# Kernel tuning notes

Measured on AMD Instinct MI355X. Metric: run time of the kernel, lower is better.

Reference implementation:

```python
import jax, jax.numpy as jnp
import numpy as np

N_USER = 100000
N_ITEM = 100000
SUPP = 10000
B = 1024
L = 50
S = 256
H = 4
E = 64
HID = 64


def setup_inputs() -> dict:
    key = jax.random.key(0)
    ks = jax.random.split(key, 32)
    f32 = jnp.float32
    inp = {}
    # forward int args
    inp["x"] = jax.random.randint(ks[0], (B, 2), 0, N_USER)
    inp["src_his"] = jax.random.randint(ks[1], (B, L), 0, N_ITEM)
    inp["src_hl"] = jax.random.randint(ks[2], (B,), 0, L)
    inp["tgt_his"] = jax.random.randint(ks[3], (B, L), 0, N_ITEM)
    inp["tgt_hl"] = jax.random.randint(ks[4], (B,), 0, L)
    # precomputed neighbor sampling: [2 get_user_emb calls, H heads, B, S]
    inp["sample_idx"] = jax.random.randint(ks[5], (2, H, B, S), 0, SUPP)
    inp["supp_users"] = jax.random.randint(ks[6], (SUPP,), 0, N_USER)
    # embedding tables (xavier-ish small scale)
    inp["src_user_emb"] = jax.random.normal(ks[7], (N_USER, E), f32) * 0.1
    inp["src_item_emb"] = jax.random.normal(ks[8], (N_ITEM, E), f32) * 0.1
    inp["tgt_user_emb"] = jax.random.normal(ks[9], (N_USER, E), f32) * 0.1
    inp["tgt_item_emb"] = jax.random.normal(ks[10], (N_ITEM, E), f32) * 0.1
    # attention / aggregation weights, stored [in, out]
    s = 1.0 / np.sqrt(E)
    inp["W_att_w"] = jax.random.normal(ks[11], (E, E), f32) * s
    inp["W_att_b"] = jnp.full((E,), 0.1, f32)
    inp["W_agg_w"] = jax.random.normal(ks[12], (E, E), f32) * s
    # per-head GAT projections, batched over heads
    inp["Wq"] = jax.random.normal(ks[13], (H, E, E), f32) * s
    inp["Wk"] = jax.random.normal(ks[14], (H, E, E), f32) * s
    inp["Wv"] = jax.random.normal(ks[15], (H, E, E), f32) * s
    inp["W_out"] = jax.random.normal(ks[16], (H * E, E), f32) * (1.0 / np.sqrt(H * E))
    # scoring MLP
    inp["l1_w"] = jax.random.normal(ks[17], (2 * E, HID), f32) * (1.0 / np.sqrt(2 * E))
    inp["l1_b"] = jnp.full((HID,), 0.1, f32)
    inp["l2_w"] = jax.random.normal(ks[18], (HID, E), f32) * (1.0 / np.sqrt(HID))
    inp["l2_b"] = jnp.full((E,), 0.1, f32)
    inp["l3_w"] = jax.random.normal(ks[19], (E, 1), f32) * s
    inp["l3_b"] = jnp.full((1,), 0.1, f32)
    return inp


def reference(x, src_his, src_hl, tgt_his, tgt_hl, sample_idx, supp_users,
              src_user_emb, src_item_emb, tgt_user_emb, tgt_item_emb,
              W_att_w, W_att_b, W_agg_w, Wq, Wk, Wv, W_out,
              l1_w, l1_b, l2_w, l2_b, l3_w, l3_b):
    user_id = x[:, 0]
    item_id = x[:, 1]

    def user_fea_encode(his, hl, user_table):
        # NOTE: original always gathers from src_model.item_embedding (even for tgt)
        Lh = his.shape[1]
        valid = jnp.arange(Lh)[None, :] < hl[:, None]          # [B,L]
        hist = src_item_emb[his] * valid[..., None]             # [B,L,E], padded rows zeroed
        u = user_table[user_id]                                 # [B,E]
        keyt = jnp.tanh(hist @ W_att_w + W_att_b)               # [B,L,E]
        pad = hist.sum(-1) == 0                                 # [B,L]
        att = jnp.einsum('ble,be->bl', keyt, u)
        # faithful masked_softmax: masked scores set to 0 BEFORE exp (exp(0)=1 still contributes)
        att = jnp.where(pad, 0.0, att)
        e = jnp.exp(att)
        att = e / (jnp.sum(e, axis=1, keepdims=True) + 1e-12)
        out = jnp.einsum('bl,ble->be', att, hist)
        return out @ W_agg_w                                    # W_agg has no bias

    def get_user_emb(fea, idx):
        # idx: [H,B,S] indices into supp_users; all heads batched in one einsum chain
        neigh = tgt_user_emb[supp_users[idx]]                   # [H,B,S,E]
        q = jnp.einsum('be,heo->hbo', fea, Wq)                  # [H,B,O]
        k = jnp.einsum('hbse,heo->hbso', neigh, Wk)             # [H,B,S,O]
        attn = jax.nn.softmax(jnp.einsum('hbo,hbso->hbs', q, k), axis=-1)
        ctx = jnp.einsum('hbs,hbso->hbo', attn, k)              # weighted sum over neighbors
        g = jnp.einsum('hbo,hop->hbp', ctx, Wv)                 # [H,B,O]
        g = jnp.transpose(g, (1, 0, 2)).reshape(fea.shape[0], -1)  # concat heads -> [B,H*O]
        return g @ W_out

    user_src_fea = user_fea_encode(src_his, src_hl, src_user_emb)
    user_emb = get_user_emb(user_src_fea, sample_idx[0])
    item_emb = tgt_item_emb[item_id]
    user_tgt_fea = user_fea_encode(tgt_his, tgt_hl, tgt_user_emb)
    hybrid_tgt_emb = get_user_emb(user_tgt_fea, sample_idx[1])

    x_t = jnp.concatenate([hybrid_tgt_emb, item_emb], axis=1)
    x1_t = jnp.tanh(x_t @ l1_w + l1_b)
    x2_t = jnp.tanh(x1_t @ l2_w + l2_b)
    x3_t = (x2_t @ l3_w + l3_b).reshape(-1)

    output = jnp.sum(user_emb * item_emb, axis=1)
    out_emb_s = user_emb * item_emb
    # (output, output_t, out_emb_s, out_emb_t); train=False branch (sim/domain heads are None)
    return (output, x3_t, out_emb_s, x2_t)
```

## Files before the change

kernel.cpp:

```cpp
#include <hip/hip_runtime.h>

constexpr int B    = 1024;
constexpr int L    = 50;
constexpr int S    = 256;
constexpr int H    = 4;
constexpr int E    = 64;
constexpr int HID  = 64;
constexpr int SUPP = 10000;

__device__ __forceinline__ float tanh_fast(float x) {
    const float xc = fminf(fmaxf(x, -15.0f), 15.0f);
    const float e  = __expf(2.0f * xc);
    return (e - 1.0f) * __builtin_amdgcn_rcpf(e + 1.0f);
}

__global__ __launch_bounds__(256) void pre_kernel(
    const int* __restrict__ x,
    const int* __restrict__ src_his,
    const int* __restrict__ src_hl,
    const int* __restrict__ tgt_his,
    const int* __restrict__ tgt_hl,
    const float* __restrict__ item_emb,
    const float* __restrict__ src_user_emb,
    const float* __restrict__ tgt_user_emb,
    const int* __restrict__ supp_users,
    const float* __restrict__ W_att_w,
    const float* __restrict__ W_att_b,
    const float* __restrict__ W_agg_w,
    const float* __restrict__ Wq,
    const float* __restrict__ Wk,
    float* __restrict__ qout,
    float* __restrict__ K_supp)
{
    const int tid  = threadIdx.x;
    const int lane = tid & 63;
    const int wave = tid >> 6;

    if (blockIdx.y == 2) {
        __shared__ __align__(16) float sEv[4][E];
        const int h = wave;
        float wkc[E];
#pragma unroll
        for (int i = 0; i < E; i++) wkc[i] = Wk[h * E * E + i * E + lane];

        for (int j0 = blockIdx.x * 4; j0 < SUPP; j0 += gridDim.x * 4) {
            const int jm = j0 + wave;
            if (jm < SUPP) {
                const int u = supp_users[jm];
                sEv[wave][lane] = tgt_user_emb[(size_t)u * E + lane];
            }
            __syncthreads();
            const int mmax = min(4, SUPP - j0);
            for (int m = 0; m < mmax; m++) {
                const float4* e4 = (const float4*)&sEv[m][0];
                float a0 = 0.0f, a1 = 0.0f, a2 = 0.0f, a3 = 0.0f;
#pragma unroll
                for (int k = 0; k < 16; k++) {
                    const float4 v = e4[k];
                    a0 += v.x * wkc[4 * k + 0];
                    a1 += v.y * wkc[4 * k + 1];
                    a2 += v.z * wkc[4 * k + 2];
                    a3 += v.w * wkc[4 * k + 3];
                }
                K_supp[((size_t)h * SUPP + j0 + m) * E + lane] = (a0 + a1) + (a2 + a3);
            }
            __syncthreads();
        }
        return;
    }

    __shared__ __align__(16) float sHist[L * E];
    __shared__ float sHs[L];
    __shared__ float sAtt[L];
    __shared__ float sPart[4][E];
    __shared__ __align__(16) float sOut[E];
    __shared__ __align__(16) float sFea[E];

    const int b    = blockIdx.x;
    const int call = blockIdx.y;

    const int* his = call ? tgt_his : src_his;
    const int* hl  = call ? tgt_hl  : src_hl;
    const float* user_table = call ? tgt_user_emb : src_user_emb;

    float wcol[E];
#pragma unroll
    for (int i = 0; i < E; i++) wcol[i] = W_att_w[i * E + lane];

    const int uid    = x[2 * b];
    const float uv   = user_table[(size_t)uid * E + lane];
    const float bias = W_att_b[lane];
    const int hlen   = hl[b];

    for (int l = wave; l < L; l += 4) {
        const int it = his[b * L + l];
        const float hv = (l < hlen) ? item_emb[(size_t)it * E + lane] : 0.0f;
        sHist[l * E + lane] = hv;
        float hs = hv;
#pragma unroll
        for (int off = 32; off; off >>= 1) hs += __shfl_xor(hs, off);
        if (lane == 0) sHs[l] = hs;
    }
    __syncthreads();

    for (int l = wave; l < L; l += 4) {
        const float4* hrow = (const float4*)&sHist[l * E];
        float a0 = 0.0f, a1 = 0.0f, a2 = 0.0f, a3 = 0.0f;
#pragma unroll
        for (int k = 0; k < 16; k++) {
            const float4 h4 = hrow[k];
            a0 += h4.x * wcol[4 * k + 0];
            a1 += h4.y * wcol[4 * k + 1];
            a2 += h4.z * wcol[4 * k + 2];
            a3 += h4.w * wcol[4 * k + 3];
        }
        float part = tanh_fast((a0 + a1) + (a2 + a3) + bias) * uv;
#pragma unroll
        for (int off = 32; off; off >>= 1) part += __shfl_xor(part, off);
        const float hs = sHs[l];
        if (lane == 0) sAtt[l] = (hs == 0.0f) ? 0.0f : part;
    }
    __syncthreads();

    if (wave == 0) {
        float v = (lane < L) ? __expf(sAtt[lane]) : 0.0f;
        float s = v;
#pragma unroll
        for (int off = 32; off; off >>= 1) s += __shfl_xor(s, off);
        const float denom = s + 1e-12f;
        if (lane < L) sAtt[lane] = v / denom;
    }
    __syncthreads();

    float c = 0.0f;
    for (int l = wave; l < L; l += 4) c += sAtt[l] * sHist[l * E + lane];
    sPart[wave][lane] = c;
    __syncthreads();
    if (tid < E) sOut[tid] = sPart[0][tid] + sPart[1][tid] + sPart[2][tid] + sPart[3][tid];
    __syncthreads();

    {
        const float4* o4 = (const float4*)&sOut[wave * 16];
        float g0 = 0.0f, g1 = 0.0f, g2 = 0.0f, g3 = 0.0f;
#pragma unroll
        for (int k = 0; k < 4; k++) {
            const float4 v = o4[k];
            const int i = wave * 16 + 4 * k;
            g0 += v.x * W_agg_w[(i + 0) * E + lane];
            g1 += v.y * W_agg_w[(i + 1) * E + lane];
            g2 += v.z * W_agg_w[(i + 2) * E + lane];
            g3 += v.w * W_agg_w[(i + 3) * E + lane];
        }
        sPart[wave][lane] = (g0 + g1) + (g2 + g3);
    }
    __syncthreads();
    if (tid < E) sFea[tid] = sPart[0][tid] + sPart[1][tid] + sPart[2][tid] + sPart[3][tid];
    __syncthreads();

    {
        const float* Wqh = Wq + wave * E * E;
        const float4* f4p = (const float4*)sFea;
        float q0 = 0.0f, q1 = 0.0f, q2 = 0.0f, q3 = 0.0f;
#pragma unroll
        for (int k = 0; k < 16; k++) {
            const float4 f4 = f4p[k];
            q0 += f4.x * Wqh[(4 * k + 0) * E + lane];
            q1 += f4.y * Wqh[(4 * k + 1) * E + lane];
            q2 += f4.z * Wqh[(4 * k + 2) * E + lane];
            q3 += f4.w * Wqh[(4 * k + 3) * E + lane];
        }
        qout[(((call * H) + wave) * B + b) * E + lane] = (q0 + q1) + (q2 + q3);
    }
}

__global__ __launch_bounds__(256) void attn_kernel(
    const int* __restrict__ sample_idx,
    const float* __restrict__ K_supp,
    const float* __restrict__ qarr,
    const float* __restrict__ Wv,
    float* __restrict__ gout)
{
    __shared__ float sRed[8];
    __shared__ float sCtx[4][E];
    __shared__ float sC[E];
    __shared__ float sG[4][E];

    const int n    = blockIdx.x;
    const int xcd  = n & 7;
    const int h    = xcd >> 1;
    const int call = xcd & 1;
    const int b    = n >> 3;
    const int tid  = threadIdx.x;
    const int lane = tid & 63;
    const int wave = tid >> 6;
    const int u    = lane & 15;
    const int rsub = lane >> 4;
    const int s0   = wave * 64;

    const int* idx = sample_idx + (((call * H) + h) * B + b) * S;
    const float* Kh = K_supp + (size_t)h * SUPP * E;
    const float4 qu = *(const float4*)(qarr + ((size_t)(((call * H) + h) * B + b)) * E + 4 * u);

    float4 kreg[16];
    float mylogit = 0.0f;
#pragma unroll
    for (int i = 0; i < 16; i++) {
        const int j = idx[s0 + 4 * i + rsub];
        kreg[i] = *(const float4*)(Kh + (size_t)j * E + 4 * u);
        float part = kreg[i].x * qu.x + kreg[i].y * qu.y
                   + kreg[i].z * qu.z + kreg[i].w * qu.w;
#pragma unroll
        for (int off = 1; off < 16; off <<= 1) part += __shfl_xor(part, off);
        mylogit = (u == i) ? part : mylogit;
    }

    float m = mylogit;
#pragma unroll
    for (int off = 32; off; off >>= 1) m = fmaxf(m, __shfl_xor(m, off));
    if (lane == 0) sRed[wave] = m;
    __syncthreads();
    const float mx = fmaxf(fmaxf(sRed[0], sRed[1]), fmaxf(sRed[2], sRed[3]));
    const float ex = __expf(mylogit - mx);
    float sm = ex;
#pragma unroll
    for (int off = 32; off; off >>= 1) sm += __shfl_xor(sm, off);
    if (lane == 0) sRed[4 + wave] = sm;
    __syncthreads();
    const float denom = sRed[4] + sRed[5] + sRed[6] + sRed[7];
    const float pval = ex / denom;

    float4 cacc = make_float4(0.0f, 0.0f, 0.0f, 0.0f);
#pragma unroll
    for (int i = 0; i < 16; i++) {
        const float p = __shfl(pval, (lane & 48) + i);
        cacc.x += p * kreg[i].x;
        cacc.y += p * kreg[i].y;
        cacc.z += p * kreg[i].z;
        cacc.w += p * kreg[i].w;
    }
#pragma unroll
    for (int off = 16; off <= 32; off <<= 1) {
        cacc.x += __shfl_xor(cacc.x, off);
        cacc.y += __shfl_xor(cacc.y, off);
        cacc.z += __shfl_xor(cacc.z, off);
        cacc.w += __shfl_xor(cacc.w, off);
    }
    if (lane < 16) *(float4*)(&sCtx[wave][u * 4]) = cacc;
    __syncthreads();
    if (wave == 0) {
        sC[lane] = sCtx[0][lane] + sCtx[1][lane] + sCtx[2][lane] + sCtx[3][lane];
    }
    __syncthreads();

    const float* Wvh = Wv + h * E * E;
    float g = 0.0f;
#pragma unroll
    for (int k = 0; k < 16; k++) {
        const int c = wave * 16 + k;
        g += sC[c] * Wvh[c * E + lane];
    }
    sG[wave][lane] = g;
    __syncthreads();
    if (wave == 0) {
        gout[((size_t)(call * B) + b) * (H * E) + h * E + lane] =
            sG[0][lane] + sG[1][lane] + sG[2][lane] + sG[3][lane];
    }
}

__global__ __launch_bounds__(256) void final_kernel(
    const int* __restrict__ x,
    const float* __restrict__ tgt_item_emb,
    const float* __restrict__ gsrc,
    const float* __restrict__ gtgt,
    const float* __restrict__ W_out,
    const float* __restrict__ l1_w,
    const float* __restrict__ l1_b,
    const float* __restrict__ l2_w,
    const float* __restrict__ l2_b,
    const float* __restrict__ l3_w,
    const float* __restrict__ l3_b,
    float* __restrict__ out)
{
    __shared__ float sPart[4][E];
    __shared__ float sHyb[E];
    __shared__ float sItem[E];
    __shared__ float sX1[HID];

    const int b    = blockIdx.x;
    const int tid  = threadIdx.x;
    const int lane = tid & 63;
    const int wave = tid >> 6;

    if (tid < E) {
        const int item = x[2 * b + 1];
        sItem[tid] = tgt_item_emb[(size_t)item * E + tid];
    }

    const float* grow = (wave < 2) ? (gsrc + (size_t)b * (H * E))
                                   : (gtgt + (size_t)b * (H * E));
    const int i0 = (wave & 1) * 128;
    {
        const float4* g4 = (const float4*)(grow + i0);
        float a0 = 0.0f, a1 = 0.0f, a2 = 0.0f, a3 = 0.0f;
#pragma unroll
        for (int k = 0; k < 32; k++) {
            const float4 v = g4[k];
            const float* wr = W_out + (i0 + 4 * k) * E + lane;
            a0 += v.x * wr[0];
            a1 += v.y * wr[E];
            a2 += v.z * wr[2 * E];
            a3 += v.w * wr[3 * E];
        }
        sPart[wave][lane] = (a0 + a1) + (a2 + a3);
    }
    __syncthreads();

    if (wave == 0) {
        const float ue = sPart[0][lane] + sPart[1][lane];
        const float prod = ue * sItem[lane];
        out[2 * B + b * E + lane] = prod;
        float s = prod;
#pragma unroll
        for (int off = 32; off; off >>= 1) s += __shfl_xor(s, off);
        if (lane == 0) out[b] = s;
    }
    if (wave == 1) {
        sHyb[lane] = sPart[2][lane] + sPart[3][lane];
    }
    __syncthreads();

    float a1 = 0.0f;
#pragma unroll
    for (int k = 0; k < 32; k++) {
        const int i = wave * 32 + k;
        const float v = (i < 64) ? sHyb[i] : sItem[i - 64];
        a1 += v * l1_w[i * HID + lane];
    }
    sPart[wave][lane] = a1;
    __syncthreads();

    if (wave == 0) {
        const float a = l1_b[lane] + sPart[0][lane] + sPart[1][lane]
                      + sPart[2][lane] + sPart[3][lane];
        sX1[lane] = tanh_fast(a);
    }
    __syncthreads();

    if (wave == 0) {
        float a = l2_b[lane];
#pragma unroll
        for (int i = 0; i < HID; i++) a += sX1[i] * l2_w[i * E + lane];
        const float x2 = tanh_fast(a);
        out[2 * B + B * E + b * E + lane] = x2;
        float p = x2 * l3_w[lane];
#pragma unroll
        for (int off = 32; off; off >>= 1) p += __shfl_xor(p, off);
        if (lane == 0) out[B + b] = p + l3_b[0];
    }
}

extern "C" void kernel_launch(void* const* d_in, const int* in_sizes, int n_in,
                              void* d_out, int out_size, void* d_ws, size_t ws_size,
                              hipStream_t stream) {
    const int*   x            = (const int*)d_in[0];
    const int*   src_his      = (const int*)d_in[1];
    const int*   src_hl       = (const int*)d_in[2];
    const int*   tgt_his      = (const int*)d_in[3];
    const int*   tgt_hl       = (const int*)d_in[4];
    const int*   sample_idx   = (const int*)d_in[5];
    const int*   supp_users   = (const int*)d_in[6];
    const float* src_user_emb = (const float*)d_in[7];
    const float* src_item_emb = (const float*)d_in[8];
    const float* tgt_user_emb = (const float*)d_in[9];
    const float* tgt_item_emb = (const float*)d_in[10];
    const float* W_att_w      = (const float*)d_in[11];
    const float* W_att_b      = (const float*)d_in[12];
    const float* W_agg_w      = (const float*)d_in[13];
    const float* Wq           = (const float*)d_in[14];
    const float* Wk           = (const float*)d_in[15];
    const float* Wv           = (const float*)d_in[16];
    const float* W_out        = (const float*)d_in[17];
    const float* l1_w         = (const float*)d_in[18];
    const float* l1_b         = (const float*)d_in[19];
    const float* l2_w         = (const float*)d_in[20];
    const float* l2_b         = (const float*)d_in[21];
    const float* l3_w         = (const float*)d_in[22];
    const float* l3_b         = (const float*)d_in[23];

    float* ws      = (float*)d_ws;
    float* qarr    = ws;
    float* K_supp  = qarr + 2 * H * B * E;
    float* garr    = K_supp + H * SUPP * E;
    float* out     = (float*)d_out;

    pre_kernel<<<dim3(B, 3), 256, 0, stream>>>(
        x, src_his, src_hl, tgt_his, tgt_hl, src_item_emb,
        src_user_emb, tgt_user_emb, supp_users,
        W_att_w, W_att_b, W_agg_w, Wq, Wk, qarr, K_supp);
    attn_kernel<<<dim3(B * H * 2), 256, 0, stream>>>(
        sample_idx, K_supp, qarr, Wv, garr);
    final_kernel<<<dim3(B), 256, 0, stream>>>(
        x, tgt_item_emb, garr, garr + B * H * E, W_out,
        l1_w, l1_b, l2_w, l2_b, l3_w, l3_b, out);
}
```

Baseline: 259.4 us.

## Register-block projections across rows and batch gathers for memory-level parallelism

After: 688.0 us. +165.2%, slower.

```diff
diff --git a/kernel.cpp b/kernel.cpp
--- a/kernel.cpp
+++ b/kernel.cpp
@@ -7,11 +7,17 @@
 constexpr int E    = 64;
 constexpr int HID  = 64;
 constexpr int SUPP = 10000;
+constexpr int RW   = 13;
+constexpr int LP   = 52;
 
 __device__ __forceinline__ float tanh_fast(float x) {
     const float xc = fminf(fmaxf(x, -15.0f), 15.0f);
     const float e  = __expf(2.0f * xc);
     return (e - 1.0f) * __builtin_amdgcn_rcpf(e + 1.0f);
+}
+
+__device__ __forceinline__ float lanebc(float v, int l) {
+    return __int_as_float(__builtin_amdgcn_readlane(__float_as_int(v), l));
 }
 
 __global__ __launch_bounds__(256) void pre_kernel(
@@ -37,41 +43,43 @@
     const int wave = tid >> 6;
 
     if (blockIdx.y == 2) {
-        __shared__ __align__(16) float sEv[4][E];
+        __shared__ __align__(16) float sEv[8][E];
         const int h = wave;
-        float wkc[E];
-#pragma unroll
-        for (int i = 0; i < E; i++) wkc[i] = Wk[h * E * E + i * E + lane];
-
-        for (int j0 = blockIdx.x * 4; j0 < SUPP; j0 += gridDim.x * 4) {
-            const int jm = j0 + wave;
-            if (jm < SUPP) {
-                const int u = supp_users[jm];
-                sEv[wave][lane] = tgt_user_emb[(size_t)u * E + lane];
+        const float* Wkh = Wk + h * E * E;
+
+        for (int j0 = blockIdx.x * 8; j0 < SUPP; j0 += gridDim.x * 8) {
+#pragma unroll
+            for (int t = 0; t < 2; t++) {
+                const int jm = j0 + 2 * wave + t;
+                if (jm < SUPP) {
+                    const int u = supp_users[jm];
+                    sEv[2 * wave + t][lane] = tgt_user_emb[(size_t)u * E + lane];
+                }
             }
             __syncthreads();
-            const int mmax = min(4, SUPP - j0);
-            for (int m = 0; m < mmax; m++) {
-                const float4* e4 = (const float4*)&sEv[m][0];
-                float a0 = 0.0f, a1 = 0.0f, a2 = 0.0f, a3 = 0.0f;
-#pragma unroll
-                for (int k = 0; k < 16; k++) {
-                    const float4 v = e4[k];
-                    a0 += v.x * wkc[4 * k + 0];
-                    a1 += v.y * wkc[4 * k + 1];
-                    a2 += v.z * wkc[4 * k + 2];
-                    a3 += v.w * wkc[4 * k + 3];
+
+            float acc[8] = {0.f, 0.f, 0.f, 0.f, 0.f, 0.f, 0.f, 0.f};
+#pragma unroll
+            for (int k = 0; k < 16; k++) {
+                const float* wp = Wkh + (4 * k) * E + lane;
+                const float w0 = wp[0], w1 = wp[E], w2 = wp[2 * E], w3 = wp[3 * E];
+#pragma unroll
+                for (int m = 0; m < 8; m++) {
+                    const float4 v = *(const float4*)&sEv[m][4 * k];
+                    acc[m] = fmaf(v.w, w3, fmaf(v.z, w2, fmaf(v.y, w1, fmaf(v.x, w0, acc[m]))));
                 }
-                K_supp[((size_t)h * SUPP + j0 + m) * E + lane] = (a0 + a1) + (a2 + a3);
             }
+            const int mmax = min(8, SUPP - j0);
+            for (int m = 0; m < mmax; m++)
+                K_supp[((size_t)h * SUPP + j0 + m) * E + lane] = acc[m];
             __syncthreads();
         }
         return;
     }
 
-    __shared__ __align__(16) float sHist[L * E];
-    __shared__ float sHs[L];
-    __shared__ float sAtt[L];
+    __shared__ __align__(16) float sHist[LP * E];
+    __shared__ float sHs[LP];
+    __shared__ float sAtt[LP];
     __shared__ float sPart[4][E];
     __shared__ __align__(16) float sOut[E];
     __shared__ __align__(16) float sFea[E];
@@ -82,58 +90,64 @@
     const int* his = call ? tgt_his : src_his;
     const int* hl  = call ? tgt_hl  : src_hl;
     const float* user_table = call ? tgt_user_emb : src_user_emb;
-
-    float wcol[E];
-#pragma unroll
-    for (int i = 0; i < E; i++) wcol[i] = W_att_w[i * E + lane];
 
     const int uid    = x[2 * b];
     const float uv   = user_table[(size_t)uid * E + lane];
     const float bias = W_att_b[lane];
     const int hlen   = hl[b];
 
-    for (int l = wave; l < L; l += 4) {
-        const int it = his[b * L + l];
-        const float hv = (l < hlen) ? item_emb[(size_t)it * E + lane] : 0.0f;
-        sHist[l * E + lane] = hv;
-        float hs = hv;
+    float hvv[RW];
+#pragma unroll
+    for (int r = 0; r < RW; r++) {
+        const int l  = wave + 4 * r;
+        const int it = (l < L) ? his[b * L + l] : 0;
+        hvv[r] = (l < hlen) ? item_emb[(size_t)it * E + lane] : 0.0f;
+    }
+#pragma unroll
+    for (int r = 0; r < RW; r++) {
+        const int l = wave + 4 * r;
+        sHist[l * E + lane] = hvv[r];
+        float hs = hvv[r];
 #pragma unroll
         for (int off = 32; off; off >>= 1) hs += __shfl_xor(hs, off);
         if (lane == 0) sHs[l] = hs;
     }
     __syncthreads();
 
-    for (int l = wave; l < L; l += 4) {
-        const float4* hrow = (const float4*)&sHist[l * E];
-        float a0 = 0.0f, a1 = 0.0f, a2 = 0.0f, a3 = 0.0f;
-#pragma unroll
-        for (int k = 0; k < 16; k++) {
-            const float4 h4 = hrow[k];
-            a0 += h4.x * wcol[4 * k + 0];
-            a1 += h4.y * wcol[4 * k + 1];
-            a2 += h4.z * wcol[4 * k + 2];
-            a3 += h4.w * wcol[4 * k + 3];
+    float acc[RW] = {0.f, 0.f, 0.f, 0.f, 0.f, 0.f, 0.f, 0.f, 0.f, 0.f, 0.f, 0.f, 0.f};
+#pragma unroll
+    for (int k = 0; k < 16; k++) {
+        const float* wp = W_att_w + (4 * k) * E + lane;
+        const float w0 = wp[0], w1 = wp[E], w2 = wp[2 * E], w3 = wp[3 * E];
+#pragma unroll
+        for (int r = 0; r < RW; r++) {
+            const float4 h4 = *(const float4*)&sHist[(wave + 4 * r) * E + 4 * k];
+            acc[r] = fmaf(h4.w, w3, fmaf(h4.z, w2, fmaf(h4.y, w1, fmaf(h4.x, w0, acc[r]))));
         }
-        float part = tanh_fast((a0 + a1) + (a2 + a3) + bias) * uv;
+    }
+#pragma unroll
+    for (int r = 0; r < RW; r++) {
+        const int l = wave + 4 * r;
+        float part = tanh_fast(acc[r] + bias) * uv;
 #pragma unroll
         for (int off = 32; off; off >>= 1) part += __shfl_xor(part, off);
-        const float hs = sHs[l];
-        if (lane == 0) sAtt[l] = (hs == 0.0f) ? 0.0f : part;
-    }
-    __syncthreads();
-
-    if (wave == 0) {
-        float v = (lane < L) ? __expf(sAtt[lane]) : 0.0f;
-        float s = v;
-#pragma unroll
-        for (int off = 32; off; off >>= 1) s += __shfl_xor(s, off);
-        const float denom = s + 1e-12f;
-        if (lane < L) sAtt[lane] = v / denom;
-    }
-    __syncthreads();
+        if (lane == 0 && l < L) sAtt[l] = (sHs[l] == 0.0f) ? 0.0f : part;
+    }
+    __syncthreads();
+
+    const float vex = (lane < L) ? __expf(sAtt[lane]) : 0.0f;
+    float sden = vex;
+#pragma unroll
+    for (int off = 32; off; off >>= 1) sden += __shfl_xor(sden, off);
+    const float rden = __builtin_amdgcn_rcpf(sden + 1e-12f);
 
     float c = 0.0f;
-    for (int l = wave; l < L; l += 4) c += sAtt[l] * sHist[l * E + lane];
+#pragma unroll
+    for (int r = 0; r < RW; r++) {
+        const int l = wave + 4 * r;
+        const float p = lanebc(vex, l) * rden;
+        c = fmaf(p, sHist[l * E + lane], c);
+    }
     sPart[wave][lane] = c;
     __syncthreads();
     if (tid < E) sOut[tid] = sPart[0][tid] + sPart[1][tid] + sPart[2][tid] + sPart[3][tid];
@@ -145,11 +159,11 @@
 #pragma unroll
         for (int k = 0; k < 4; k++) {
             const float4 v = o4[k];
-            const int i = wave * 16 + 4 * k;
-            g0 += v.x * W_agg_w[(i + 0) * E + lane];
-            g1 += v.y * W_agg_w[(i + 1) * E + lane];
-            g2 += v.z * W_agg_w[(i + 2) * E + lane];
-            g3 += v.w * W_agg_w[(i + 3) * E + lane];
+            const float* wr = W_agg_w + (wave * 16 + 4 * k) * E + lane;
+            g0 += v.x * wr[0];
+            g1 += v.y * wr[E];
+            g2 += v.z * wr[2 * E];
+            g3 += v.w * wr[3 * E];
         }
         sPart[wave][lane] = (g0 + g1) + (g2 + g3);
     }
@@ -164,10 +178,11 @@
 #pragma unroll
         for (int k = 0; k < 16; k++) {
             const float4 f4 = f4p[k];
-            q0 += f4.x * Wqh[(4 * k + 0) * E + lane];
-            q1 += f4.y * Wqh[(4 * k + 1) * E + lane];
-            q2 += f4.z * Wqh[(4 * k + 2) * E + lane];
-            q3 += f4.w * Wqh[(4 * k + 3) * E + lane];
+            const float* wr = Wqh + (4 * k) * E + lane;
+            q0 += f4.x * wr[0];
+            q1 += f4.y * wr[E];
+            q2 += f4.z * wr[2 * E];
+            q3 += f4.w * wr[3 * E];
         }
         qout[(((call * H) + wave) * B + b) * E + lane] = (q0 + q1) + (q2 + q3);
     }
@@ -201,12 +216,17 @@
     const float* Kh = K_supp + (size_t)h * SUPP * E;
     const float4 qu = *(const float4*)(qarr + ((size_t)(((call * H) + h) * B + b)) * E + 4 * u);
 
+    int jr[16];
+#pragma unroll
+    for (int i = 0; i < 16; i++) jr[i] = idx[s0 + 4 * i + rsub];
     float4 kreg[16];
+#pragma unroll
+    for (int i = 0; i < 16; i++)
+        kreg[i] = *(const float4*)(Kh + (size_t)jr[i] * E + 4 * u);
+
     float mylogit = 0.0f;
 #pragma unroll
     for (int i = 0; i < 16; i++) {
-        const int j = idx[s0 + 4 * i + rsub];
-        kreg[i] = *(const float4*)(Kh + (size_t)j * E + 4 * u);
         float part = kreg[i].x * qu.x + kreg[i].y * qu.y
                    + kreg[i].z * qu.z + kreg[i].w * qu.w;
 #pragma unroll
```
